# Performance work log

Hardware: AMD Instinct MI355X
Metric: run time of the kernel (lower is better)

## Reference

```python
import jax, jax.numpy as jnp
import numpy as np

D_MODEL = 192
NODE_NUM = 64
DEPTH = 2
ALPHA = 0.05
NUM_LAYERS = 2
LN_EPS = 1e-5


def _gcn(x, p):
    # x: [N, in_dim*D_MODEL]; faithful port of GCN.forward (eval mode)
    nv1, nv2, ws, bs, wm, bm, we, be, wl, bl, g, b = p
    N = x.shape[0]
    in_dim = x.shape[1] // D_MODEL
    adp = jax.nn.softmax(jax.nn.relu(nv1 @ nv2), axis=1)            # [V,V]
    adj = adp + jnp.eye(NODE_NUM, dtype=x.dtype)
    a = adj / adj.sum(1, keepdims=True)                              # row-normalized
    h0 = jax.lax.conv_general_dilated(
        x.reshape(N, in_dim, D_MODEL), ws, (1,), 'VALID',
        dimension_numbers=('NCH', 'OIH', 'NCH')) + bs[None, :, None]  # [N,C,V]
    h = h0
    outs = [h0]
    for _ in range(DEPTH):
        h = ALPHA * h0 + (1.0 - ALPHA) * jnp.einsum('ncw,vw->ncv', h, a)
        outs.append(h)
    ho = jnp.concatenate(outs, axis=1)                               # [N,(DEPTH+1)C,V]
    ho = jax.nn.gelu(jnp.einsum('ncv,oc->nov', ho, wm) + bm[None, :, None], approximate=False)
    ho = jnp.einsum('ncv,oc->nov', ho, we) + be[None, :, None]       # [N,6,V]
    ho = jnp.einsum('nov,dv->nod', ho, wl) + bl                      # [N,6,D]
    mu = ho.mean(-1, keepdims=True)
    var = ((ho - mu) ** 2).mean(-1, keepdims=True)                   # biased, like torch LN
    ho = (ho - mu) / jnp.sqrt(var + LN_EPS) * g + b
    return ho.reshape(N, 6 * D_MODEL)


def _encoder(inp4, flag, layer_params):
    x = jnp.transpose(inp4, (2, 0, 1, 3)) if flag == 1 else jnp.transpose(inp4, (1, 0, 2, 3))
    W, B, O, D = x.shape
    L = W + O - 1
    N = W * B
    # input_transfer: shift row r by r along the slice axis
    place = jax.vmap(lambda xr, r: jax.lax.dynamic_update_slice(
        jnp.zeros((B, L, D), x.dtype), xr, (0, r, 0)))
    a = place(x, jnp.arange(W)).reshape(N, L, D)
    layer0_output = None
    output_all = None
    rows_layers, cols_layers = [], []
    for layer in range(NUM_LAYERS):
        if layer >= 1:
            a = output_all  # eval mode: F.dropout is identity
            if layer == 1:
                layer0_output = a
        p = layer_params[layer]

        def step(carry, x_t, p=p):
            h_row, h_col = carry
            gate = _gcn(jnp.concatenate([h_row, h_col, x_t], axis=-1), p)  # [N,6D]
            sg = jax.nn.sigmoid(gate[:, :4 * D])
            tg = jnp.tanh(gate[:, 4 * D:])
            ug_r, og_r, ug_c, og_c = jnp.split(sg, 4, axis=-1)
            ig_r, ig_c = jnp.split(tg, 2, axis=-1)
            h_row = jnp.tanh((1.0 - ug_r) * h_row + ug_r * ig_r) * og_r
            h_col = jnp.tanh((1.0 - ug_c) * h_col + ug_c * ig_c) * og_c
            out_s = jnp.concatenate([h_row, h_col], axis=-1)
            # col hidden is saved pre-roll, rolled for next step
            return (h_row, jnp.roll(h_col, B, axis=0)), (out_s, h_row, h_col)

        init = (jnp.zeros((N, D), x.dtype), jnp.zeros((N, D), x.dtype))
        _, (outs, hrows, hcols) = jax.lax.scan(step, init, jnp.swapaxes(a, 0, 1))
        output_all = jnp.swapaxes(outs, 0, 1)                        # [N,L,2D]
        if layer >= 1:
            output_all = output_all + layer0_output
        # rows saved at slice s>=O-1 from block loc = s-O+1
        rows = hrows.reshape(L, W, B, D)[jnp.arange(O - 1, L), jnp.arange(W)]  # [W,B,D]
        # cols saved at slice s>=W-1 from last batch block
        cols = hcols[W - 1:, (W - 1) * B:, :]                        # [O,B,D]
        rows_layers.append(rows)
        cols_layers.append(cols)
    hidden_row_all = jnp.stack(rows_layers).transpose(2, 0, 1, 3)    # [B,layers,W,D]
    hidden_col_all = jnp.stack(cols_layers).transpose(2, 0, 1, 3)    # [B,layers,O,D]
    if flag == 1:
        return output_all, hidden_col_all, hidden_row_all
    return output_all, hidden_row_all, hidden_col_all


def setup_inputs() -> dict:
    key = jax.random.key(0)
    ks = jax.random.split(key, 20)
    idx = [0]
    def nxt():
        k = ks[idx[0]]
        idx[0] += 1
        return k
    B, W, O = 8, 24, 48
    K = D_MODEL - NODE_NUM + 1  # 129
    cc, sc, nd = 16, 32, 40
    d = {"input": jax.random.normal(nxt(), (B, W, O, D_MODEL), dtype=jnp.float32)}
    for li, in_dim in enumerate([3, 4]):
        d[f"nodevec1_{li}"] = jax.random.normal(nxt(), (NODE_NUM, nd), dtype=jnp.float32)
        d[f"nodevec2_{li}"] = jax.random.normal(nxt(), (nd, NODE_NUM), dtype=jnp.float32)
        d[f"w_start_{li}"] = jax.random.normal(nxt(), (cc, in_dim, K), dtype=jnp.float32) * 0.05
        d[f"b_start_{li}"] = jnp.zeros((cc,), jnp.float32)
        d[f"w_mlp_{li}"] = jax.random.normal(nxt(), (sc, (DEPTH + 1) * cc), dtype=jnp.float32) * 0.05
        d[f"b_mlp_{li}"] = jnp.zeros((sc,), jnp.float32)
        d[f"w_end_{li}"] = jax.random.normal(nxt(), (6, sc), dtype=jnp.float32) * 0.05
        d[f"b_end_{li}"] = jnp.zeros((6,), jnp.float32)
        d[f"w_lin_{li}"] = jax.random.normal(nxt(), (D_MODEL, NODE_NUM), dtype=jnp.float32) * 0.05
        d[f"b_lin_{li}"] = jnp.zeros((D_MODEL,), jnp.float32)
        d[f"gamma_{li}"] = jnp.ones((D_MODEL,), jnp.float32)
        d[f"beta_{li}"] = jnp.zeros((D_MODEL,), jnp.float32)
    d["flag"] = 0
    return d


def reference(input, nodevec1_0, nodevec2_0, w_start_0, b_start_0, w_mlp_0, b_mlp_0,
              w_end_0, b_end_0, w_lin_0, b_lin_0, gamma_0, beta_0,
              nodevec1_1, nodevec2_1, w_start_1, b_start_1, w_mlp_1, b_mlp_1,
              w_end_1, b_end_1, w_lin_1, b_lin_1, gamma_1, beta_1, flag):
    p0 = (nodevec1_0, nodevec2_0, w_start_0, b_start_0, w_mlp_0, b_mlp_0,
          w_end_0, b_end_0, w_lin_0, b_lin_0, gamma_0, beta_0)
    p1 = (nodevec1_1, nodevec2_1, w_start_1, b_start_1, w_mlp_1, b_mlp_1,
          w_end_1, b_end_1, w_lin_1, b_lin_1, gamma_1, beta_1)
    return _encoder(input, flag, (p0, p1))
```

## Files before the change

### kernel.cpp

```cpp
#include <hip/hip_runtime.h>
#include <hip/hip_bf16.h>

#define NT 512
typedef unsigned short u16;

__device__ __forceinline__ u16 tobf(float x) {
  union { __hip_bfloat16 h; u16 u; } cv;
  cv.h = __float2bfloat16(x);
  return cv.u;
}
__device__ __forceinline__ float frombf(u16 u) {
  return __uint_as_float(((unsigned)u) << 16);
}
__device__ __forceinline__ float sigf(float x) {
  return __builtin_amdgcn_rcpf(1.f + __builtin_amdgcn_exp2f(-1.4426950408889634f * x));
}
__device__ __forceinline__ float tanh_fast(float x) {
  return 1.f - 2.f * __builtin_amdgcn_rcpf(1.f + __builtin_amdgcn_exp2f(2.8853900817779268f * x));
}
__device__ __forceinline__ void lds_fence() {
  asm volatile("s_waitcnt lgkmcnt(0)" ::: "memory");
  __builtin_amdgcn_sched_barrier(0);
}

struct SeqArgs {
  const float* input;
  const float* nv1_0; const float* nv2_0; const float* nv1_1; const float* nv2_1;
  const float* w_start0; const float* b_start0; const float* w_mlp0; const float* b_mlp0;
  const float* w_end0;   const float* b_end0;   const float* w_lin0; const float* b_lin0;
  const float* gamma0;   const float* beta0;
  const float* w_start1; const float* b_start1; const float* w_mlp1; const float* b_mlp1;
  const float* w_end1;   const float* b_end1;   const float* w_lin1; const float* b_lin1;
  const float* gamma1;   const float* beta1;
  float* HCOL;
  int*   flags;
  float* out_all; float* out_hrow; float* out_hcol;
};

__global__ __launch_bounds__(NT, 2) void seq_kernel(SeqArgs A) {
  const int n = blockIdx.x, w = n >> 3, b = n & 7, tid = threadIdx.x;
  const int pred = (n + 184) % 192;

  __shared__ __align__(16) float sCIN[768];
  __shared__ __align__(16) u16   sWS[64 * 132];
  __shared__ __align__(16) float sAT[4096];
  __shared__ __align__(16) float sH[2][1024];
  __shared__ __align__(16) float sAbuf[4928];
  float* const sPart = sAbuf;
  float* const sG    = sAbuf;
  float* const sH2c  = sAbuf + 2048;
  float* const sE    = sAbuf + 2048;
  float* const sY    = sAbuf;
  float* const smWE  = sAbuf + 3072;
  float* const smBE  = sAbuf + 3264;
  float* const smWM  = sAbuf + 3328;

  for (int layer = 0; layer < 2; ++layer) {
    const int in_dim = 3 + layer;
    const int P = in_dim - 1;
    const float* nv1    = layer ? A.nv1_1    : A.nv1_0;
    const float* nv2    = layer ? A.nv2_1    : A.nv2_0;
    const float* wstart = layer ? A.w_start1 : A.w_start0;
    const float* bs     = layer ? A.b_start1 : A.b_start0;
    const float* wm     = layer ? A.w_mlp1   : A.w_mlp0;
    const float* bm     = layer ? A.b_mlp1   : A.b_mlp0;
    const float* we     = layer ? A.w_end1   : A.w_end0;
    const float* be     = layer ? A.b_end1   : A.b_end0;
    const float* wl     = layer ? A.w_lin1   : A.w_lin0;
    const float* bl     = layer ? A.b_lin1   : A.b_lin0;
    const float* gm     = layer ? A.gamma1   : A.gamma0;
    const float* bt     = layer ? A.beta1    : A.beta0;

    for (int idx = tid; idx < 4096; idx += NT) {
      int v = idx >> 6, ww = idx & 63;
      float s = 0.f;
      for (int j = 0; j < 40; ++j) s = fmaf(nv1[v*40 + j], nv2[j*64 + ww], s);
      sAbuf[idx] = fmaxf(s, 0.f);
    }
    __syncthreads();
    if (tid < 64) {
      const int v = tid;
      float m = -1e30f;
      for (int ww = 0; ww < 64; ++ww) m = fmaxf(m, sAbuf[v*64 + ww]);
      float s = 0.f;
      for (int ww = 0; ww < 64; ++ww) { float e = expf(sAbuf[v*64 + ww] - m); sAbuf[v*64 + ww] = e; s += e; }
      float inv = 1.f / s, rs = 1.f;
      for (int ww = 0; ww < 64; ++ww) rs += sAbuf[v*64 + ww] * inv;
      float irs = 1.f / rs;
      for (int ww = 0; ww < 64; ++ww) {
        float a = sAbuf[v*64 + ww] * inv + ((ww == v) ? 1.f : 0.f);
        sAT[ww*64 + v] = a * irs;
      }
    }
    __syncthreads();
    for (int idx = tid; idx < 16*in_dim*132; idx += NT) {
      int row = idx / 132, k = idx - row*132;
      sWS[idx] = (k < 129) ? tobf(wstart[((row & 15)*in_dim + (row >> 4))*129 + k]) : (u16)0;
    }
    for (int idx = tid; idx < 1536; idx += NT) { int o = idx/48, c = idx - o*48; smWM[o*50 + c] = wm[idx]; }
    for (int idx = tid; idx < 192; idx += NT) smWE[idx] = we[idx];
    if (tid < 6) smBE[tid] = be[tid];
    for (int d = tid; d < 384; d += NT) sCIN[d] = 0.f;

    const int v_p = tid & 63;
    const int o0  = tid >> 6;
    const float bmv0 = bm[o0], bmv1 = bm[o0 + 8], bmv2 = bm[o0 + 16], bmv3 = bm[o0 + 24];
    float blv = 0.f, gmv = 1.f, btv = 0.f;
    if (tid < 384) blv = bl[(tid >= 192) ? tid - 192 : tid];
    if (tid < 192) { gmv = gm[tid]; btv = bt[tid]; }
    float bs_r[2];
    bs_r[0] = bs[tid >> 6];
    bs_r[1] = bs[(tid >> 6) + 8];
    __syncthreads();

    auto pre_phase = [&](int t) {
      if (layer == 0) {
        int o = t - w;
        if (o >= 0 && o < 48) {
          const float* xr = A.input + (((size_t)(b*24 + w)*48 + o)*192);
          for (int d = tid; d < 192; d += NT) sCIN[384 + d] = xr[d];
        } else {
          for (int d = tid; d < 192; d += NT) sCIN[384 + d] = 0.f;
        }
      } else {
        const float* xr = A.out_all + ((size_t)n*71 + t)*384;
        for (int d = tid; d < 384; d += NT) sCIN[384 + d] = xr[d];
      }
      __syncthreads();
      const int nslots = P << 8;
      for (int s = tid; s < nslots; s += NT) {
        const int cidx = s >> 4;
        const int p = cidx >> 4, c = cidx & 15;
        const int vg = s & 15;
        const int ich = (p == 0) ? 0 : (p + 1);
        const float* xin = ((p == 0) ? &sCIN[0] : &sCIN[384 + (p-1)*192]) + vg*4;
        const u16* wrow = &sWS[(ich*16 + c)*132];
        float a0 = 0.f, a1 = 0.f, a2 = 0.f, a3 = 0.f;
        float4 xc = *(const float4*)xin;
        for (int k4 = 0; k4 < 128; k4 += 4) {
          ushort4 wu = *(const ushort4*)(wrow + k4);
          float w0 = frombf(wu.x), w1 = frombf(wu.y), w2 = frombf(wu.z), w3 = frombf(wu.w);
          float4 xn = *(const float4*)(xin + k4 + 4);
          a0 = fmaf(w3, xc.w, fmaf(w2, xc.z, fmaf(w1, xc.y, fmaf(w0, xc.x, a0))));
          a1 = fmaf(w3, xn.x, fmaf(w2, xc.w, fmaf(w1, xc.z, fmaf(w0, xc.y, a1))));
          a2 = fmaf(w3, xn.y, fmaf(w2, xn.x, fmaf(w1, xc.w, fmaf(w0, xc.z, a2))));
          a3 = fmaf(w3, xn.z, fmaf(w2, xn.y, fmaf(w1, xn.x, fmaf(w0, xc.w, a3))));
          xc = xn;
        }
        float wk = frombf(wrow[128]);
        a0 = fmaf(wk, xc.x, a0); a1 = fmaf(wk, xc.y, a1);
        a2 = fmaf(wk, xc.z, a2); a3 = fmaf(wk, xc.w, a3);
        *(float4*)&sPart[cidx*64 + vg*4] = make_float4(a0, a1, a2, a3);
      }
      __syncthreads();
      {
        const int c0 = tid >> 6, v = tid & 63;
        float sum0 = bs_r[0], sum1 = bs_r[1];
        for (int p = 0; p < P; ++p) {
          sum0 += sPart[(p*16 + c0     )*64 + v];
          sum1 += sPart[(p*16 + c0 + 8 )*64 + v];
        }
        sH[0][ c0      *64 + v] = sum0;
        sH[0][(c0 + 8 )*64 + v] = sum1;
      }
      __syncthreads();
    };
    pre_phase(0);

    for (int t = 0; t < 71; ++t) {
      const int S = layer*71 + t;

      if (t > 0) {
        if (tid < 192) {
          while (__hip_atomic_load(&A.flags[pred*32], __ATOMIC_RELAXED, __HIP_MEMORY_SCOPE_AGENT) < S)
            __builtin_amdgcn_s_sleep(1);
          __builtin_amdgcn_sched_barrier(0);
          asm volatile("" ::: "memory");
          const float* hc = A.HCOL + ((size_t)((S-1) & 31)*192 + pred)*192;
          sCIN[192 + tid] = __hip_atomic_load(&hc[tid], __ATOMIC_RELAXED, __HIP_MEMORY_SCOPE_AGENT);
        }
        __syncthreads();
      }

      {
        const int c = tid >> 5, vg2 = tid & 31;
        const int vbase = c*64 + vg2*2;
        const float* xin = &sCIN[192 + vg2*2];
        const u16* wrow = &sWS[(16 + c)*132];
        float a0 = sH[0][vbase], a1 = sH[0][vbase + 1];
        float2 xc = *(const float2*)xin;
        for (int k2 = 0; k2 < 128; k2 += 2) {
          ushort2 wu = *(const ushort2*)(wrow + k2);
          float w0 = frombf(wu.x), w1 = frombf(wu.y);
          float2 xn = *(const float2*)(xin + k2 + 2);
          a0 = fmaf(w1, xc.y, fmaf(w0, xc.x, a0));
          a1 = fmaf(w1, xn.x, fmaf(w0, xc.y, a1));
          xc = xn;
        }
        float wk = frombf(wrow[128]);
        a0 = fmaf(wk, xc.x, a0); a1 = fmaf(wk, xc.y, a1);
        sH[0][vbase] = a0; sH[0][vbase + 1] = a1;
      }
      lds_fence();
      {
        const int c0 = o0 * 2;
        float pa0 = 0.f, pa1 = 0.f;
        for (int w4 = 0; w4 < 64; w4 += 4) {
          float a0v = sAT[(w4+0)*64 + v_p];
          float a1v = sAT[(w4+1)*64 + v_p];
          float a2v = sAT[(w4+2)*64 + v_p];
          float a3v = sAT[(w4+3)*64 + v_p];
          float4 h0v = *(const float4*)&sH[0][ c0      *64 + w4];
          float4 h1v = *(const float4*)&sH[0][(c0 + 1 )*64 + w4];
          pa0 = fmaf(h0v.x, a0v, pa0); pa0 = fmaf(h0v.y, a1v, pa0);
          pa0 = fmaf(h0v.z, a2v, pa0); pa0 = fmaf(h0v.w, a3v, pa0);
          pa1 = fmaf(h1v.x, a0v, pa1); pa1 = fmaf(h1v.y, a1v, pa1);
          pa1 = fmaf(h1v.z, a2v, pa1); pa1 = fmaf(h1v.w, a3v, pa1);
        }
        float h0a = sH[0][ c0      *64 + v_p];
        float h0b = sH[0][(c0 + 1 )*64 + v_p];
        sH[1][ c0      *64 + v_p] = fmaf(0.95f, pa0, 0.05f * h0a);
        sH[1][(c0 + 1 )*64 + v_p] = fmaf(0.95f, pa1, 0.05f * h0b);
        lds_fence();
        float pb0 = 0.f, pb1 = 0.f;
        for (int w4 = 0; w4 < 64; w4 += 4) {
          float a0v = sAT[(w4+0)*64 + v_p];
          float a1v = sAT[(w4+1)*64 + v_p];
          float a2v = sAT[(w4+2)*64 + v_p];
          float a3v = sAT[(w4+3)*64 + v_p];
          float4 h0v = *(const float4*)&sH[1][ c0      *64 + w4];
          float4 h1v = *(const float4*)&sH[1][(c0 + 1 )*64 + w4];
          pb0 = fmaf(h0v.x, a0v, pb0); pb0 = fmaf(h0v.y, a1v, pb0);
          pb0 = fmaf(h0v.z, a2v, pb0); pb0 = fmaf(h0v.w, a3v, pb0);
          pb1 = fmaf(h1v.x, a0v, pb1); pb1 = fmaf(h1v.y, a1v, pb1);
          pb1 = fmaf(h1v.z, a2v, pb1); pb1 = fmaf(h1v.w, a3v, pb1);
        }
        sH2c[ c0      *64 + v_p] = fmaf(0.95f, pb0, 0.05f * h0a);
        sH2c[(c0 + 1 )*64 + v_p] = fmaf(0.95f, pb1, 0.05f * h0b);
      }
      __syncthreads();

      {
        float g0 = bmv0, g1 = bmv1, g2 = bmv2, g3 = bmv3;
#pragma unroll
        for (int c = 0; c < 16; ++c) {
          float h0v = sH[0][c*64 + v_p];
          float h1v = sH[1][c*64 + v_p];
          float h2v = sH2c[c*64 + v_p];
          g0 = fmaf(smWM[(o0     )*50 + c], h0v, fmaf(smWM[(o0     )*50 + 16 + c], h1v, fmaf(smWM[(o0     )*50 + 32 + c], h2v, g0)));
          g1 = fmaf(smWM[(o0 +  8)*50 + c], h0v, fmaf(smWM[(o0 +  8)*50 + 16 + c], h1v, fmaf(smWM[(o0 +  8)*50 + 32 + c], h2v, g1)));
          g2 = fmaf(smWM[(o0 + 16)*50 + c], h0v, fmaf(smWM[(o0 + 16)*50 + 16 + c], h1v, fmaf(smWM[(o0 + 16)*50 + 32 + c], h2v, g2)));
          g3 = fmaf(smWM[(o0 + 24)*50 + c], h0v, fmaf(smWM[(o0 + 24)*50 + 16 + c], h1v, fmaf(smWM[(o0 + 24)*50 + 32 + c], h2v, g3)));
        }
        g0 = 0.5f * g0 * (1.f + erff(g0 * 0.70710678118654752f));
        g1 = 0.5f * g1 * (1.f + erff(g1 * 0.70710678118654752f));
        g2 = 0.5f * g2 * (1.f + erff(g2 * 0.70710678118654752f));
        g3 = 0.5f * g3 * (1.f + erff(g3 * 0.70710678118654752f));
        sG[(o0     )*64 + v_p] = g0;
        sG[(o0 +  8)*64 + v_p] = g1;
        sG[(o0 + 16)*64 + v_p] = g2;
        sG[(o0 + 24)*64 + v_p] = g3;
      }
      __syncthreads();

      for (int idx = tid; idx < 384; idx += NT) {
        int o2 = idx >> 6, v = idx & 63;
        float acc = smBE[o2];
        for (int c = 0; c < 32; ++c) acc = fmaf(smWE[o2*32 + c], sG[c*64 + v], acc);
        sE[idx] = acc;
      }
      __syncthreads();

      if (tid < 384) {
        const int d  = (tid >= 192) ? tid - 192 : tid;
        const int r0 = (tid >= 192) ? 3 : 0;
        const float4* wrow = (const float4*)(wl + d*64);
        float y0 = blv, y1 = blv, y2 = blv;
        for (int q = 0; q < 16; ++q) {
          float4 wv = wrow[q];
          float4 e0 = *(const float4*)&sE[(r0+0)*64 + q*4];
          float4 e1 = *(const float4*)&sE[(r0+1)*64 + q*4];
          float4 e2 = *(const float4*)&sE[(r0+2)*64 + q*4];
          y0 = fmaf(e0.x,wv.x, fmaf(e0.y,wv.y, fmaf(e0.z,wv.z, fmaf(e0.w,wv.w, y0))));
          y1 = fmaf(e1.x,wv.x, fmaf(e1.y,wv.y, fmaf(e1.z,wv.z, fmaf(e1.w,wv.w, y1))));
          y2 = fmaf(e2.x,wv.x, fmaf(e2.y,wv.y, fmaf(e2.z,wv.z, fmaf(e2.w,wv.w, y2))));
        }
        sY[(r0+0)*192 + d] = y0;
        sY[(r0+1)*192 + d] = y1;
        sY[(r0+2)*192 + d] = y2;
      }
      __syncthreads();

      if (tid < 192) {
        const int r = tid >> 5, l32 = tid & 31;
        float sm = 0.f, sq = 0.f;
#pragma unroll
        for (int m = 0; m < 6; ++m) {
          float v = sY[r*192 + l32 + 32*m];
          sm += v; sq = fmaf(v, v, sq);
        }
#pragma unroll
        for (int off = 16; off >= 1; off >>= 1) {
          sm += __shfl_xor(sm, off);
          sq += __shfl_xor(sq, off);
        }
        if (l32 == 0) {
          float mu = sm * (1.f/192.f);
          float var = sq * (1.f/192.f) - mu*mu;
          sH[1][r] = mu;
          sH[1][8 + r] = rsqrtf(fmaxf(var, 0.f) + 1e-5f);
        }
      }
      __syncthreads();

      float hcn = 0.f;
      if (tid < 192) {
        const int d = tid;
        float y2 = fmaf((sY[2*192+d] - sH[1][2]) * sH[1][10], gmv, btv);
        float y3 = fmaf((sY[3*192+d] - sH[1][3]) * sH[1][11], gmv, btv);
        float y5 = fmaf((sY[5*192+d] - sH[1][5]) * sH[1][13], gmv, btv);
        float ugc = sigf(y2), ogc = sigf(y3), igc = tanh_fast(y5);
        float hc = sCIN[192 + d];
        hcn = tanh_fast(fmaf(ugc, igc, (1.f - ugc)*hc)) * ogc;
        __hip_atomic_store(&A.HCOL[((size_t)(S & 31)*192 + n)*192 + d], hcn,
                           __ATOMIC_RELAXED, __HIP_MEMORY_SCOPE_AGENT);
      }
      __syncthreads();
      if (tid == 0) {
        asm volatile("s_waitcnt vmcnt(0)" ::: "memory");
        __hip_atomic_store(&A.flags[n*32], S + 1, __ATOMIC_RELAXED, __HIP_MEMORY_SCOPE_AGENT);
      }
      if (tid < 192) {
        const int d = tid;
        float y0 = fmaf((sY[0*192+d] - sH[1][0]) * sH[1][8],  gmv, btv);
        float y1 = fmaf((sY[1*192+d] - sH[1][1]) * sH[1][9],  gmv, btv);
        float y4 = fmaf((sY[4*192+d] - sH[1][4]) * sH[1][12], gmv, btv);
        float ugr = sigf(y0), ogr = sigf(y1), igr = tanh_fast(y4);
        float hr = sCIN[d];
        float hrn = tanh_fast(fmaf(ugr, igr, (1.f - ugr)*hr)) * ogr;
        sCIN[d] = hrn;
        float* oa = A.out_all + ((size_t)n*71 + t)*384;
        if (layer == 0) { oa[d] = hrn; oa[192 + d] = hcn; }
        else           { oa[d] = hrn + sCIN[384 + d]; oa[192 + d] = hcn + sCIN[576 + d]; }
        if (t == 47 + w)
          A.out_hrow[(((size_t)b*2 + layer)*24 + w)*192 + d] = hrn;
        if (w == 23 && t >= 23)
          A.out_hcol[(((size_t)b*2 + layer)*48 + (t - 23))*192 + d] = hcn;
      }
      __syncthreads();
      if (t < 70) pre_phase(t + 1);
    }
    __syncthreads();
  }
}

extern "C" void kernel_launch(void* const* d_in, const int* in_sizes, int n_in,
                              void* d_out, int out_size, void* d_ws, size_t ws_size,
                              hipStream_t stream) {
  (void)in_sizes; (void)n_in; (void)out_size; (void)ws_size;
  char* ws = (char*)d_ws;
  int*   flags = (int*)ws;
  float* HCOL  = (float*)(ws + 24576);

  hipMemsetAsync(flags, 0, 24576, stream);

  SeqArgs A;
  A.input    = (const float*)d_in[0];
  A.nv1_0    = (const float*)d_in[1];  A.nv2_0 = (const float*)d_in[2];
  A.w_start0 = (const float*)d_in[3];  A.b_start0 = (const float*)d_in[4];
  A.w_mlp0   = (const float*)d_in[5];  A.b_mlp0   = (const float*)d_in[6];
  A.w_end0   = (const float*)d_in[7];  A.b_end0   = (const float*)d_in[8];
  A.w_lin0   = (const float*)d_in[9];  A.b_lin0   = (const float*)d_in[10];
  A.gamma0   = (const float*)d_in[11]; A.beta0    = (const float*)d_in[12];
  A.nv1_1    = (const float*)d_in[13]; A.nv2_1 = (const float*)d_in[14];
  A.w_start1 = (const float*)d_in[15]; A.b_start1 = (const float*)d_in[16];
  A.w_mlp1   = (const float*)d_in[17]; A.b_mlp1   = (const float*)d_in[18];
  A.w_end1   = (const float*)d_in[19]; A.b_end1   = (const float*)d_in[20];
  A.w_lin1   = (const float*)d_in[21]; A.b_lin1   = (const float*)d_in[22];
  A.gamma1   = (const float*)d_in[23]; A.beta1    = (const float*)d_in[24];
  A.HCOL = HCOL; A.flags = flags;
  A.out_all  = (float*)d_out;
  A.out_hrow = (float*)d_out + 5234688;
  A.out_hcol = (float*)d_out + 5308416;

  seq_kernel<<<192, NT, 0, stream>>>(A);
}
```

Baseline: 2.707 ms.

## Replace flag handshake with sequence-tagged 64-bit column-state exchange and lighter barriers

Each column-state value is stored as a 64-bit word tagged with its step number, so consumers poll the data itself. This removes the separate flag store, its vmcnt wait and the extra block barrier on the critical cross-block chain. A successor progress counter throttles the 16-slot ring so producers cannot overwrite slots that are still unread. Next-step input loads are issued early into registers to overlap global latency, and __syncthreads is replaced by a raw s_barrier after an LDS wait. The costs are twice the HCOL traffic and a larger memset, and the raw barriers do not wait for outstanding global memory operations.

```diff
diff --git a/kernel.cpp b/kernel.cpp
--- a/kernel.cpp
+++ b/kernel.cpp
@@ -3,6 +3,7 @@
 
 #define NT 512
 typedef unsigned short u16;
+typedef unsigned long long u64;
 
 __device__ __forceinline__ u16 tobf(float x) {
   union { __hip_bfloat16 h; u16 u; } cv;
@@ -21,6 +22,11 @@
 __device__ __forceinline__ void lds_fence() {
   asm volatile("s_waitcnt lgkmcnt(0)" ::: "memory");
   __builtin_amdgcn_sched_barrier(0);
+}
+__device__ __forceinline__ void bar_light() {
+  asm volatile("s_waitcnt lgkmcnt(0)" ::: "memory");
+  __builtin_amdgcn_s_barrier();
+  asm volatile("" ::: "memory");
 }
 
 struct SeqArgs {
@@ -32,14 +38,15 @@
   const float* w_start1; const float* b_start1; const float* w_mlp1; const float* b_mlp1;
   const float* w_end1;   const float* b_end1;   const float* w_lin1; const float* b_lin1;
   const float* gamma1;   const float* beta1;
-  float* HCOL;
-  int*   flags;
+  u64*   HCOL2;
+  int*   prog;
   float* out_all; float* out_hrow; float* out_hcol;
 };
 
 __global__ __launch_bounds__(NT, 2) void seq_kernel(SeqArgs A) {
   const int n = blockIdx.x, w = n >> 3, b = n & 7, tid = threadIdx.x;
   const int pred = (n + 184) % 192;
+  const int succ = (n + 8) % 192;
 
   __shared__ __align__(16) float sCIN[768];
   __shared__ __align__(16) u16   sWS[64 * 132];
@@ -113,20 +120,7 @@
     bs_r[1] = bs[(tid >> 6) + 8];
     __syncthreads();
 
-    auto pre_phase = [&](int t) {
-      if (layer == 0) {
-        int o = t - w;
-        if (o >= 0 && o < 48) {
-          const float* xr = A.input + (((size_t)(b*24 + w)*48 + o)*192);
-          for (int d = tid; d < 192; d += NT) sCIN[384 + d] = xr[d];
-        } else {
-          for (int d = tid; d < 192; d += NT) sCIN[384 + d] = 0.f;
-        }
-      } else {
-        const float* xr = A.out_all + ((size_t)n*71 + t)*384;
-        for (int d = tid; d < 384; d += NT) sCIN[384 + d] = xr[d];
-      }
-      __syncthreads();
+    auto pre_conv = [&]() {
       const int nslots = P << 8;
       for (int s = tid; s < nslots; s += NT) {
         const int cidx = s >> 4;
@@ -152,7 +146,7 @@
         a2 = fmaf(wk, xc.z, a2); a3 = fmaf(wk, xc.w, a3);
         *(float4*)&sPart[cidx*64 + vg*4] = make_float4(a0, a1, a2, a3);
       }
-      __syncthreads();
+      bar_light();
       {
         const int c0 = tid >> 6, v = tid & 63;
         float sum0 = bs_r[0], sum1 = bs_r[1];
@@ -163,23 +157,62 @@
         sH[0][ c0      *64 + v] = sum0;
         sH[0][(c0 + 8 )*64 + v] = sum1;
       }
-      __syncthreads();
+      bar_light();
     };
-    pre_phase(0);
+
+    {
+      if (layer == 0) {
+        int o = 0 - w;
+        if (o >= 0 && o < 48) {
+          const float* xr = A.input + (((size_t)(b*24 + w)*48 + o)*192);
+          for (int d = tid; d < 192; d += NT) sCIN[384 + d] = xr[d];
+        } else {
+          for (int d = tid; d < 192; d += NT) sCIN[384 + d] = 0.f;
+        }
+      } else {
+        const float* xr = A.out_all + ((size_t)n*71 + 0)*384;
+        for (int d = tid; d < 384; d += NT) sCIN[384 + d] = xr[d];
+      }
+      bar_light();
+      pre_conv();
+    }
 
     for (int t = 0; t < 71; ++t) {
       const int S = layer*71 + t;
 
+      float xpa = 0.f, xpb = 0.f;
+      if (t < 70 && tid < 192) {
+        if (layer == 0) {
+          int o = (t + 1) - w;
+          if (o >= 0 && o < 48)
+            xpa = A.input[(((size_t)(b*24 + w)*48 + o)*192) + tid];
+        } else {
+          const float* xr = A.out_all + ((size_t)n*71 + (t+1))*384;
+          xpa = xr[tid];
+          xpb = xr[192 + tid];
+        }
+      }
+
       if (t > 0) {
         if (tid < 192) {
-          while (__hip_atomic_load(&A.flags[pred*32], __ATOMIC_RELAXED, __HIP_MEMORY_SCOPE_AGENT) < S)
-            __builtin_amdgcn_s_sleep(1);
-          __builtin_amdgcn_sched_barrier(0);
-          asm volatile("" ::: "memory");
-          const float* hc = A.HCOL + ((size_t)((S-1) & 31)*192 + pred)*192;
-          sCIN[192 + tid] = __hip_atomic_load(&hc[tid], __ATOMIC_RELAXED, __HIP_MEMORY_SCOPE_AGENT);
-        }
-        __syncthreads();
+          const u64* src = &A.HCOL2[((size_t)((S-1) & 15)*192 + pred)*192 + tid];
+          u64 v;
+          do {
+            v = __hip_atomic_load(src, __ATOMIC_RELAXED, __HIP_MEMORY_SCOPE_AGENT);
+          } while ((unsigned)(v >> 32) != (unsigned)S);
+          sCIN[192 + tid] = __uint_as_float((unsigned)v);
+        } else if (tid == 256 && S >= 16) {
+          while (__hip_atomic_load(&A.prog[succ*32], __ATOMIC_RELAXED, __HIP_MEMORY_SCOPE_AGENT) < S - 15)
+            __builtin_amdgcn_s_sleep(2);
+        }
+        bar_light();
+        if (tid == 0)
+          __hip_atomic_store(&A.prog[n*32], S, __ATOMIC_RELAXED, __HIP_MEMORY_SCOPE_AGENT);
+      } else if (S >= 16) {
+        if (tid == 256) {
+          while (__hip_atomic_load(&A.prog[succ*32], __ATOMIC_RELAXED, __HIP_MEMORY_SCOPE_AGENT) < S - 15)
+            __builtin_amdgcn_s_sleep(2);
+        }
       }
 
       {
@@ -238,7 +271,7 @@
         sH2c[ c0      *64 + v_p] = fmaf(0.95f, pb0, 0.05f * h0a);
         sH2c[(c0 + 1 )*64 + v_p] = fmaf(0.95f, pb1, 0.05f * h0b);
       }
-      __syncthreads();
+      bar_light();
 
       {
         float g0 = bmv0, g1 = bmv1, g2 = bmv2, g3 = bmv3;
@@ -261,7 +294,7 @@
         sG[(o0 + 16)*64 + v_p] = g2;
         sG[(o0 + 24)*64 + v_p] = g3;
       }
-      __syncthreads();
+      bar_light();
 
       for (int idx = tid; idx < 384; idx += NT) {
         int o2 = idx >> 6, v = idx & 63;
@@ -269,7 +302,7 @@
         for (int c = 0; c < 32; ++c) acc = fmaf(smWE[o2*32 + c], sG[c*64 + v], acc);
         sE[idx] = acc;
       }
-      __syncthreads();
+      bar_light();
 
       if (tid < 384) {
         const int d  = (tid >= 192) ? tid - 192 : tid;
@@ -289,7 +322,7 @@
         sY[(r0+1)*192 + d] = y1;
         sY[(r0+2)*192 + d] = y2;
       }
-      __syncthreads();
+      bar_light();
 
       if (tid < 192) {
         const int r = tid >> 5, l32 = tid & 31;
@@ -311,7 +344,7 @@
           sH[1][8 + r] = rsqrtf(fmaxf(var, 0.f) + 1e-5f);
         }
       }
-      __syncthreads();
+      bar_light();
 
       float hcn = 0.f;
       if (tid < 192) {
@@ -322,13 +355,9 @@
         float ugc = sigf(y2), ogc = sigf(y3), igc = tanh_fast(y5);
         float hc = sCIN[192 + d];
         hcn = tanh_fast(fmaf(ugc, igc, (1.f - ugc)*hc)) * ogc;
-        __hip_atomic_store(&A.HCOL[((size_t)(S & 31)*192 + n)*192 + d], hcn,
+        u64 pk = ((u64)(unsigned)(S + 1) << 32) | (u64)__float_as_uint(hcn);
+        __hip_atomic_store(&A.HCOL2[((size_t)(S & 15)*192 + n)*192 + d], pk,
                            __ATOMIC_RELAXED, __HIP_MEMORY_SCOPE_AGENT);
-      }
-      __syncthreads();
-      if (tid == 0) {
-        asm volatile("s_waitcnt vmcnt(0)" ::: "memory");
-        __hip_atomic_store(&A.flags[n*32], S + 1, __ATOMIC_RELAXED, __HIP_MEMORY_SCOPE_AGENT);
       }
       if (tid < 192) {
         const int d = tid;
@@ -346,9 +375,13 @@
           A.out_hrow[(((size_t)b*2 + layer)*24 + w)*192 + d] = hrn;
         if (w == 23 && t >= 23)
           A.out_hcol[(((size_t)b*2 + layer)*48 + (t - 23))*192 + d] = hcn;
-      }
-      __syncthreads();
-      if (t < 70) pre_phase(t + 1);
+        if (t < 70) {
+          sCIN[384 + d] = xpa;
+          if (layer == 1) sCIN[576 + d] = xpb;
+        }
+      }
+      bar_light();
+      if (t < 70) pre_conv();
     }
     __syncthreads();
   }
@@ -359,10 +392,10 @@
                               hipStream_t stream) {
   (void)in_sizes; (void)n_in; (void)out_size; (void)ws_size;
   char* ws = (char*)d_ws;
-  int*   flags = (int*)ws;
-  float* HCOL  = (float*)(ws + 24576);
-
-  hipMemsetAsync(flags, 0, 24576, stream);
+  int* prog  = (int*)ws;
+  u64* HCOL2 = (u64*)(ws + 24576);
+
+  hipMemsetAsync(ws, 0, 24576 + 4718592, stream);
 
   SeqArgs A;
   A.input    = (const float*)d_in[0];
@@ -378,7 +411,7 @@
   A.w_end1   = (const float*)d_in[19]; A.b_end1   = (const float*)d_in[20];
   A.w_lin1   = (const float*)d_in[21]; A.b_lin1   = (const float*)d_in[22];
   A.gamma1   = (const float*)d_in[23]; A.beta1    = (const float*)d_in[24];
-  A.HCOL = HCOL; A.flags = flags;
+  A.HCOL2 = HCOL2; A.prog = prog;
   A.out_all  = (float*)d_out;
   A.out_hrow = (float*)d_out + 5234688;
   A.out_hcol = (float*)d_out + 5308416;
```

Measured after the change: 2.644 ms. 1.02x faster.
